# Kernel tuning notes

Measured on AMD Instinct MI355X. Metric: run time of the kernel, lower is better.

The kernel has to match this reference:

```python
import jax, jax.numpy as jnp
import numpy as np

B, W, F_IN = 128, 128, 64   # batch, window_size, num_features
N = 64                      # nodes per graph == num_features == tcn_out_channels
E = 4096                    # edges per graph
ED = 16                     # edge_feature_dim
H, C = 4, 32                # heads, gat_out_dim
FLAT = N * H * C            # 8192
HID = FLAT // 4             # 2048
LRELU_SLOPE = 0.01          # F.leaky_relu default
BN_EPS = 1e-5


def setup_inputs() -> dict:
    key = jax.random.key(0)
    ks = jax.random.split(key, 16)
    x = jax.random.normal(ks[0], (B, W, F_IN), jnp.float32)
    edge_index = jax.random.randint(ks[1], (2, E), 0, N)
    edge_attr = jax.random.normal(ks[2], (B, E, ED), jnp.float32)
    s = lambda k, shape, fan: jax.random.normal(k, shape, jnp.float32) / np.sqrt(fan)
    tcn_w = s(ks[3], (N, F_IN, 3), F_IN * 3)
    tcn_b = jnp.zeros((N,), jnp.float32)
    lin_l_w = s(ks[4], (H * C, W), W)
    lin_l_b = jnp.zeros((H * C,), jnp.float32)
    lin_e_w = s(ks[5], (H * C, ED), ED)
    lin_e_b = jnp.zeros((H * C,), jnp.float32)
    att = s(ks[6], (1, H, C), C)
    fc1_w = s(ks[7], (HID, FLAT), FLAT)
    fc1_b = jnp.zeros((HID,), jnp.float32)
    bn_g = jnp.ones((HID,), jnp.float32)
    bn_b = jnp.zeros((HID,), jnp.float32)
    fc2_w = s(ks[8], (2, HID), HID)
    fc2_b = jnp.zeros((2,), jnp.float32)
    return dict(x=x, edge_index=edge_index, edge_attr=edge_attr,
                tcn_w=tcn_w, tcn_b=tcn_b,
                lin_l_w=lin_l_w, lin_l_b=lin_l_b,
                lin_e_w=lin_e_w, lin_e_b=lin_e_b, att=att,
                fc1_w=fc1_w, fc1_b=fc1_b, bn_g=bn_g, bn_b=bn_b,
                fc2_w=fc2_w, fc2_b=fc2_b)


def reference(x, edge_index, edge_attr, tcn_w, tcn_b,
              lin_l_w, lin_l_b, lin_e_w, lin_e_b, att,
              fc1_w, fc1_b, bn_g, bn_b, fc2_w, fc2_b):
    # TCN: Conv1d(k=3, pad=1) over the window dim
    xt = jnp.transpose(x, (0, 2, 1))  # [B, F_IN, W]
    x_g = jax.lax.conv_general_dilated(
        xt, tcn_w, window_strides=(1,), padding=((1, 1),),
        dimension_numbers=('NCH', 'OIH', 'NCH')) + tcn_b[None, :, None]
    # x_g: [B, N, W] -> per-sample graph with N nodes, W-dim node features

    src, dst = edge_index[0], edge_index[1]

    def gat_one(xn, ea):
        # xn: [N, W], ea: [E, ED]
        h = (xn @ lin_l_w.T + lin_l_b).reshape(N, H, C)
        e = (ea @ lin_e_w.T + lin_e_b).reshape(E, H, C)
        xi = h[dst]               # [E, H, C] target node feats
        xj = h[src]               # [E, H, C] source node feats
        a = jax.nn.leaky_relu(xi + xj + e, LRELU_SLOPE)
        score = jnp.einsum('ehc,ohc->eh', a, att)  # [E, H]
        # segment softmax over edges grouped by destination node
        m = jax.ops.segment_max(score, dst, num_segments=N)
        m = jnp.where(jnp.isfinite(m), m, 0.0)
        ex = jnp.exp(score - m[dst])
        den = jax.ops.segment_sum(ex, dst, num_segments=N)
        alpha = ex / (den[dst] + 1e-16)            # [E, H]
        msg = xj * alpha[:, :, None]               # [E, H, C]
        out = jax.ops.segment_sum(msg, dst, num_segments=N)  # [N, H, C]
        return out.reshape(N, H * C)

    x_gat = jax.vmap(gat_one)(x_g, edge_attr)      # [B, N, H*C]
    x_gat = jax.nn.elu(x_gat)
    x_flat = x_gat.reshape(B, FLAT)

    h1 = x_flat @ fc1_w.T + fc1_b
    # BatchNorm1d in eval mode with fresh running stats (mean=0, var=1)
    h1 = h1 * (bn_g / jnp.sqrt(1.0 + BN_EPS)) + bn_b
    h1 = jax.nn.relu(h1)  # dropout is identity in eval
    logits = h1 @ fc2_w.T + fc2_b
    return logits
```

## Files before the change

### kernel.cpp

```cpp
#include <hip/hip_runtime.h>
#include <math.h>

#define BB   128
#define WW   128
#define FIN  64
#define NNODE 64
#define NE   4096
#define EDIM 16
#define NH   4
#define CDIM 32
#define HC   128
#define FLATD 8192
#define HIDD 2048

#define OFF_H    0u
#define OFF_P    1048576u
#define OFF_XGB  3211264u
#define OFF_BK   4259840u

typedef unsigned short u16;
typedef u16      u16x8 __attribute__((ext_vector_type(8)));
typedef __bf16   bf16x8 __attribute__((ext_vector_type(8)));
typedef float    f32x4  __attribute__((ext_vector_type(4)));
typedef float    f32x16 __attribute__((ext_vector_type(16)));

__device__ __forceinline__ u16 f2bf(float f) {
    unsigned u = __float_as_uint(f);
    u += 0x7fffu + ((u >> 16) & 1u);
    return (u16)(u >> 16);
}
__device__ __forceinline__ void hilo(float v, u16* h, u16* l) {
    u16 hh = f2bf(v);
    float hf = __uint_as_float(((unsigned)hh) << 16);
    *h = hh;
    *l = f2bf(v - hf);
}

__global__ __launch_bounds__(256) void k01(
        const float* __restrict__ x, const float* __restrict__ tcn_w,
        const float* __restrict__ tcn_b, const float* __restrict__ lin_l_w,
        const float* __restrict__ lin_l_b, float* __restrict__ h,
        const int* __restrict__ ei, int* __restrict__ bstart,
        int* __restrict__ blist)
{
    __shared__ float xs[130*65];
    __shared__ float xg[32*132];
    __shared__ float tw[32*192];
    __shared__ int cnt[64];
    __shared__ int cur[65];
    const int bid = blockIdx.x, t = threadIdx.x;

    if (bid == 256) {
        if (t < 64) cnt[t] = 0;
        __syncthreads();
        for (int e = t; e < NE; e += 256) atomicAdd(&cnt[ei[NE + e]], 1);
        __syncthreads();
        if (t == 0) {
            int run = 0;
            for (int n = 0; n < 64; ++n) { cur[n] = run; run += cnt[n]; }
            cur[64] = run;
        }
        __syncthreads();
        if (t < 65) bstart[t] = cur[t];
        __syncthreads();
        for (int e = t; e < NE; e += 256) {
            int d = ei[NE + e], s = ei[e];
            int p = atomicAdd(&cur[d], 1);
            blist[p] = (e << 12) | (d << 6) | s;
        }
        return;
    }

    const int b = bid >> 1, half = bid & 1;
    const int n0 = half * 32;

    for (int idx = t; idx < 8192; idx += 256) {
        int w = idx >> 6, i = idx & 63;
        xs[(w+1)*65 + i] = x[b*8192 + idx];
    }
    {
        const float4* src = (const float4*)(tcn_w + n0*192);
        for (int idx = t; idx < 1536; idx += 256)
            ((float4*)tw)[idx] = src[idx];
    }
    if (t < 65) { xs[t] = 0.f; xs[129*65 + t] = 0.f; }
    __syncthreads();

    {
        const int nl = t >> 3;
        const int n  = n0 + nl;
        const int w0 = (t & 7) * 16;
        float acc[16];
        const float tb = tcn_b[n];
#pragma unroll
        for (int j = 0; j < 16; ++j) acc[j] = tb;
        for (int i = 0; i < 64; ++i) {
            const float t0 = tw[nl*192 + 3*i + 0];
            const float t1 = tw[nl*192 + 3*i + 1];
            const float t2 = tw[nl*192 + 3*i + 2];
            float a = xs[(w0+0)*65 + i];
            float c0 = xs[(w0+1)*65 + i];
#pragma unroll
            for (int dw = 0; dw < 16; ++dw) {
                float c = xs[(w0+dw+2)*65 + i];
                acc[dw] += a*t0 + c0*t1 + c*t2;
                a = c0; c0 = c;
            }
        }
#pragma unroll
        for (int dw = 0; dw < 16; ++dw) xg[nl*132 + w0 + dw] = acc[dw];
    }
    __syncthreads();

    {
        const int o2 = t & 63, ng = t >> 6;
        const int oA = o2, oB = o2 + 64;
        float accA[8], accB[8];
        const float lbA = lin_l_b[oA], lbB = lin_l_b[oB];
#pragma unroll
        for (int j = 0; j < 8; ++j) { accA[j] = lbA; accB[j] = lbB; }
        for (int c = 0; c < 32; ++c) {
            const float4 lwA = *(const float4*)&lin_l_w[oA*128 + c*4];
            const float4 lwB = *(const float4*)&lin_l_w[oB*128 + c*4];
#pragma unroll
            for (int nn = 0; nn < 8; ++nn) {
                const float4 xv = *(const float4*)&xg[(ng*8+nn)*132 + c*4];
                accA[nn] += xv.x*lwA.x + xv.y*lwA.y + xv.z*lwA.z + xv.w*lwA.w;
                accB[nn] += xv.x*lwB.x + xv.y*lwB.y + xv.z*lwB.z + xv.w*lwB.w;
            }
        }
#pragma unroll
        for (int nn = 0; nn < 8; ++nn) {
            const int n = n0 + ng*8 + nn;
            h[(b*64 + n)*128 + oA] = accA[nn];
            h[(b*64 + n)*128 + oB] = accB[nn];
        }
    }
}

#define CAPF 2560
__global__ __launch_bounds__(512, 1) void k2_fused(
        const float* __restrict__ hbase, const float* __restrict__ ea,
        const float* __restrict__ lin_e_w, const float* __restrict__ lin_e_b,
        const float* __restrict__ att, const int* __restrict__ bstart,
        const int* __restrict__ blist, u16* __restrict__ xgb)
{
    __shared__ float hbuf[64*132];
    __shared__ float scl[CAPF*4];
    __shared__ float Pm[4][32][68];
    __shared__ int   bst[33];
    const int b = blockIdx.x, half = blockIdx.y, t = threadIdx.x;
    const int lane = t & 63, wv = t >> 6, l32 = lane & 31, h5 = lane >> 5;

    const int lo  = bstart[half*32];
    const int cnt = min(bstart[half*32 + 32] - lo, CAPF);
    const int gcnt = (cnt + 31) >> 5;

    int g = wv;
    int pkc = 0; bool validc = false;
    float4 v0c = {0.f,0.f,0.f,0.f}, v1c = {0.f,0.f,0.f,0.f};
    if (g < gcnt) {
        const int idx0 = g*32 + l32;
        validc = idx0 < cnt;
        pkc = validc ? blist[lo + idx0] : 0;
        const float* eap = ea + ((size_t)b*NE + (size_t)(pkc >> 12))*16 + h5*8;
        v0c = *(const float4*)eap;
        v1c = *(const float4*)(eap + 4);
    }

    for (int idx = t; idx < 2048; idx += 512) {
        const int row = idx >> 5, c4 = (idx & 31) * 4;
        float4 hv = *(const float4*)&hbase[(size_t)b*8192 + row*128 + c4];
        const float4 eb = *(const float4*)&lin_e_b[c4];
        hv.x += 0.5f*eb.x; hv.y += 0.5f*eb.y;
        hv.z += 0.5f*eb.z; hv.w += 0.5f*eb.w;
        *(float4*)&hbuf[row*132 + c4] = hv;
    }
    {
        const f32x4 z4 = {0.f, 0.f, 0.f, 0.f};
        for (int idx = t; idx < 4*32*68/4; idx += 512) ((f32x4*)Pm)[idx] = z4;
    }
    if (t < 33) bst[t] = bstart[half*32 + t];
    bf16x8 Ah[4], Al[4];
#pragma unroll
    for (int mt = 0; mt < 4; ++mt) {
        const float* wp = &lin_e_w[(mt*32 + l32)*16 + h5*8];
        const float4 w0 = *(const float4*)wp;
        const float4 w1 = *(const float4*)(wp + 4);
        u16 th[8], tl[8];
        hilo(w0.x,&th[0],&tl[0]); hilo(w0.y,&th[1],&tl[1]);
        hilo(w0.z,&th[2],&tl[2]); hilo(w0.w,&th[3],&tl[3]);
        hilo(w1.x,&th[4],&tl[4]); hilo(w1.y,&th[5],&tl[5]);
        hilo(w1.z,&th[6],&tl[6]); hilo(w1.w,&th[7],&tl[7]);
        u16x8 vh = { th[0],th[1],th[2],th[3],th[4],th[5],th[6],th[7] };
        u16x8 vl = { tl[0],tl[1],tl[2],tl[3],tl[4],tl[5],tl[6],tl[7] };
        Ah[mt] = *(bf16x8*)&vh;
        Al[mt] = *(bf16x8*)&vl;
    }
    float4 attv[4][4];
#pragma unroll
    for (int mt = 0; mt < 4; ++mt)
#pragma unroll
        for (int gq = 0; gq < 4; ++gq)
            attv[mt][gq] = *(const float4*)&att[mt*32 + gq*8 + h5*4];
    __syncthreads();

    while (g < gcnt) {
        const int gn = g + 8;
        const int pk = pkc; const bool valid = validc;
        const float4 v0 = v0c, v1 = v1c;
        const int idx = g*32 + l32;
        if (gn < gcnt) {
            const int idxn = gn*32 + l32;
            validc = idxn < cnt;
            pkc = validc ? blist[lo + idxn] : 0;
            const float* eap = ea + ((size_t)b*NE + (size_t)(pkc >> 12))*16 + h5*8;
            v0c = *(const float4*)eap;
            v1c = *(const float4*)(eap + 4);
        } else {
            validc = false;
        }
        const int sn = pk & 63, dd = (pk >> 6) & 63;
        u16 bh[8], bl[8];
        hilo(v0.x,&bh[0],&bl[0]); hilo(v0.y,&bh[1],&bl[1]);
        hilo(v0.z,&bh[2],&bl[2]); hilo(v0.w,&bh[3],&bl[3]);
        hilo(v1.x,&bh[4],&bl[4]); hilo(v1.y,&bh[5],&bl[5]);
        hilo(v1.z,&bh[6],&bl[6]); hilo(v1.w,&bh[7],&bl[7]);
        u16x8 vbh = { bh[0],bh[1],bh[2],bh[3],bh[4],bh[5],bh[6],bh[7] };
        u16x8 vbl = { bl[0],bl[1],bl[2],bl[3],bl[4],bl[5],bl[6],bl[7] };
        const bf16x8 Bh = *(bf16x8*)&vbh;
        const bf16x8 Bl = *(bf16x8*)&vbl;
        float hacc[4];
#pragma unroll
        for (int mt = 0; mt < 4; ++mt) {
            f32x16 D = {0.f,0.f,0.f,0.f,0.f,0.f,0.f,0.f,
                        0.f,0.f,0.f,0.f,0.f,0.f,0.f,0.f};
            D = __builtin_amdgcn_mfma_f32_32x32x16_bf16(Al[mt], Bh, D, 0, 0, 0);
            D = __builtin_amdgcn_mfma_f32_32x32x16_bf16(Ah[mt], Bl, D, 0, 0, 0);
            D = __builtin_amdgcn_mfma_f32_32x32x16_bf16(Ah[mt], Bh, D, 0, 0, 0);
            float s = 0.f;
#pragma unroll
            for (int g4 = 0; g4 < 4; ++g4) {
                const int ob = mt*32 + g4*8 + h5*4;
                const float4 hd = *(const float4*)&hbuf[dd*132 + ob];
                const float4 hs = *(const float4*)&hbuf[sn*132 + ob];
                float x0 = hd.x + hs.x + D[g4*4+0];
                float x1 = hd.y + hs.y + D[g4*4+1];
                float x2 = hd.z + hs.z + D[g4*4+2];
                float x3 = hd.w + hs.w + D[g4*4+3];
                x0 = fmaxf(x0, 0.01f*x0); x1 = fmaxf(x1, 0.01f*x1);
                x2 = fmaxf(x2, 0.01f*x2); x3 = fmaxf(x3, 0.01f*x3);
                const float4 a4 = attv[mt][g4];
                s += a4.x*x0 + a4.y*x1 + a4.z*x2 + a4.w*x3;
            }
            hacc[mt] = s;
        }
#pragma unroll
        for (int hh = 0; hh < 4; ++hh)
            hacc[hh] += __shfl_xor(hacc[hh], 32);
        if (h5 == 0 && valid)
            *(float4*)&scl[idx*4] = make_float4(hacc[0], hacc[1], hacc[2], hacc[3]);
        g = gn;
    }
    __syncthreads();

    {
        const int pair = t >> 2, sub = t & 3;
        const int nl = pair >> 2, hh = pair & 3;
        const int s0 = bst[nl] - lo, s1 = bst[nl+1] - lo;
        float mx = -3.4e38f;
        for (int i = s0 + sub; i < s1; i += 4) mx = fmaxf(mx, scl[i*4 + hh]);
        mx = fmaxf(mx, __shfl_xor(mx, 1));
        mx = fmaxf(mx, __shfl_xor(mx, 2));
        float den = 0.f;
        for (int i = s0 + sub; i < s1; i += 4) {
            const float ex = __expf(scl[i*4 + hh] - mx);
            scl[i*4 + hh] = ex;
            den += ex;
        }
        den += __shfl_xor(den, 1);
        den += __shfl_xor(den, 2);
        const float rd = 1.0f / (den + 1e-16f);
        for (int i = s0 + sub; i < s1; i += 4) {
            const int src = blist[lo + i] & 63;
            atomicAdd(&Pm[hh][nl][src], scl[i*4 + hh] * rd);
        }
    }
    __syncthreads();

    {
        const int hh = wv >> 1, ct = wv & 1;
        const int l16 = lane & 15, q = lane >> 4;
        const int cb = hh*32 + ct*16 + l16;
        const float lb2 = 0.5f * lin_e_b[cb];
        bf16x8 Hh2[2], Hl2[2];
#pragma unroll
        for (int kk = 0; kk < 2; ++kk) {
            u16 hhv[8], hlv[8];
#pragma unroll
            for (int i = 0; i < 8; ++i) {
                const float v = hbuf[(kk*32 + q*8 + i)*132 + cb];
                hilo(v, &hhv[i], &hlv[i]);
            }
            u16x8 vhh = { hhv[0],hhv[1],hhv[2],hhv[3],hhv[4],hhv[5],hhv[6],hhv[7] };
            u16x8 vhl = { hlv[0],hlv[1],hlv[2],hlv[3],hlv[4],hlv[5],hlv[6],hlv[7] };
            Hh2[kk] = *(bf16x8*)&vhh;
            Hl2[kk] = *(bf16x8*)&vhl;
        }
#pragma unroll
        for (int mrow = 0; mrow < 32; mrow += 16) {
            f32x4 D = {0.f, 0.f, 0.f, 0.f};
#pragma unroll
            for (int kk = 0; kk < 2; ++kk) {
                const float* pp = &Pm[hh][mrow + l16][kk*32 + q*8];
                const float4 a0 = *(const float4*)pp;
                const float4 a1 = *(const float4*)(pp + 4);
                u16 ph[8], pl[8];
                hilo(a0.x,&ph[0],&pl[0]); hilo(a0.y,&ph[1],&pl[1]);
                hilo(a0.z,&ph[2],&pl[2]); hilo(a0.w,&ph[3],&pl[3]);
                hilo(a1.x,&ph[4],&pl[4]); hilo(a1.y,&ph[5],&pl[5]);
                hilo(a1.z,&ph[6],&pl[6]); hilo(a1.w,&ph[7],&pl[7]);
                u16x8 vph = { ph[0],ph[1],ph[2],ph[3],ph[4],ph[5],ph[6],ph[7] };
                u16x8 vpl = { pl[0],pl[1],pl[2],pl[3],pl[4],pl[5],pl[6],pl[7] };
                const bf16x8 Ph = *(bf16x8*)&vph, Pl = *(bf16x8*)&vpl;
                D = __builtin_amdgcn_mfma_f32_16x16x32_bf16(Pl, Hh2[kk], D, 0, 0, 0);
                D = __builtin_amdgcn_mfma_f32_16x16x32_bf16(Ph, Hl2[kk], D, 0, 0, 0);
                D = __builtin_amdgcn_mfma_f32_16x16x32_bf16(Ph, Hh2[kk], D, 0, 0, 0);
            }
#pragma unroll
            for (int r = 0; r < 4; ++r) {
                const int m = mrow + q*4 + r;
                const float corr = (bst[m+1] > bst[m]) ? lb2 : 0.f;
                float v = D[r] - corr;
                v = v > 0.f ? v : expm1f(v);
                xgb[(size_t)b*8192 + (half*32 + m)*128 + cb] = f2bf(v);
            }
        }
    }
}

__global__ __launch_bounds__(256) void k3_fc1(
        const u16* __restrict__ xgb, const float* __restrict__ fc1_w,
        float* __restrict__ part)
{
    __shared__ u16 Ash[128*72];
    __shared__ u16 Bsh[32*72];
    const int jb = blockIdx.x, ks = blockIdx.y, t = threadIdx.x;
    const int j0 = jb*32, k0 = ks*1024;
    const int wave = t >> 6, lane = t & 63;
    const int quad = lane >> 4, l16 = lane & 15;
    const int wm = (wave & 1) * 64, wn = (wave >> 1) * 16;

    f32x4 acc[4];
#pragma unroll
    for (int i = 0; i < 4; ++i) acc[i] = (f32x4){0.f, 0.f, 0.f, 0.f};

    const int arow = t >> 1, acol = (t & 1) * 32;
    const int brow = t >> 3, bcol = (t & 7) * 8;

    u16x8 Ar[4]; float4 Br0, Br1;
    {
        const u16* ap = xgb + (size_t)arow*FLATD + k0 + acol;
#pragma unroll
        for (int qq = 0; qq < 4; ++qq) Ar[qq] = *(const u16x8*)(ap + qq*8);
        const float* bp = fc1_w + (size_t)(j0 + brow)*FLATD + k0 + bcol;
        Br0 = *(const float4*)bp; Br1 = *(const float4*)(bp + 4);
    }

    for (int kc = 0; kc < 1024; kc += 64) {
#pragma unroll
        for (int qq = 0; qq < 4; ++qq)
            *(u16x8*)&Ash[arow*72 + acol + qq*8] = Ar[qq];
        {
            u16x8 u = { f2bf(Br0.x), f2bf(Br0.y), f2bf(Br0.z), f2bf(Br0.w),
                        f2bf(Br1.x), f2bf(Br1.y), f2bf(Br1.z), f2bf(Br1.w) };
            *(u16x8*)&Bsh[brow*72 + bcol] = u;
        }
        __syncthreads();
        if (kc + 64 < 1024) {
            const u16* ap = xgb + (size_t)arow*FLATD + k0 + kc + 64 + acol;
#pragma unroll
            for (int qq = 0; qq < 4; ++qq) Ar[qq] = *(const u16x8*)(ap + qq*8);
            const float* bp = fc1_w + (size_t)(j0 + brow)*FLATD + k0 + kc + 64 + bcol;
            Br0 = *(const float4*)bp; Br1 = *(const float4*)(bp + 4);
        }
#pragma unroll
        for (int kk = 0; kk < 64; kk += 32) {
            bf16x8 af[4], bfr;
#pragma unroll
            for (int i = 0; i < 4; ++i)
                af[i] = *(const bf16x8*)&Ash[(wm + i*16 + l16)*72 + kk + quad*8];
            bfr = *(const bf16x8*)&Bsh[(wn + l16)*72 + kk + quad*8];
#pragma unroll
            for (int i = 0; i < 4; ++i)
                acc[i] = __builtin_amdgcn_mfma_f32_16x16x32_bf16(af[i], bfr, acc[i], 0, 0, 0);
        }
        __syncthreads();
    }
#pragma unroll
    for (int i = 0; i < 4; ++i) {
        const int n = j0 + wn + l16;
#pragma unroll
        for (int r = 0; r < 4; ++r) {
            const int m = wm + i*16 + quad*4 + r;
            part[(size_t)ks*262144 + (size_t)m*HIDD + n] = acc[i][r];
        }
    }
}

__global__ __launch_bounds__(256) void k4_fc2(
        const float* __restrict__ part, const float* __restrict__ fc1_b,
        const float* __restrict__ bn_g, const float* __restrict__ bn_b,
        const float* __restrict__ fc2_w, const float* __restrict__ fc2_b,
        float* __restrict__ out)
{
    __shared__ float r0[256], r1[256];
    const int b = blockIdx.x, t = threadIdx.x;
    const float inv = 1.0f / sqrtf(1.0f + 1e-5f);
    float p0 = 0.f, p1 = 0.f;
    for (int j = t; j < 2048; j += 256) {
        float hv = 0.f;
#pragma unroll
        for (int s = 0; s < 8; ++s) hv += part[(size_t)s*262144 + (size_t)b*2048 + j];
        float v = (hv + fc1_b[j]) * (bn_g[j] * inv) + bn_b[j];
        v = fmaxf(v, 0.f);
        p0 += v * fc2_w[j];
        p1 += v * fc2_w[2048 + j];
    }
    r0[t] = p0; r1[t] = p1;
    __syncthreads();
    for (int s = 128; s > 0; s >>= 1) {
        if (t < s) { r0[t] += r0[t+s]; r1[t] += r1[t+s]; }
        __syncthreads();
    }
    if (t == 0) {
        out[b*2 + 0] = r0[0] + fc2_b[0];
        out[b*2 + 1] = r1[0] + fc2_b[1];
    }
}

extern "C" void kernel_launch(void* const* d_in, const int* in_sizes, int n_in,
                              void* d_out, int out_size, void* d_ws, size_t ws_size,
                              hipStream_t stream)
{
    const float* x       = (const float*)d_in[0];
    const int*   ei      = (const int*)  d_in[1];
    const float* ea      = (const float*)d_in[2];
    const float* tcn_w   = (const float*)d_in[3];
    const float* tcn_b   = (const float*)d_in[4];
    const float* lin_l_w = (const float*)d_in[5];
    const float* lin_l_b = (const float*)d_in[6];
    const float* lin_e_w = (const float*)d_in[7];
    const float* lin_e_b = (const float*)d_in[8];
    const float* att     = (const float*)d_in[9];
    const float* fc1_w   = (const float*)d_in[10];
    const float* fc1_b   = (const float*)d_in[11];
    const float* bn_g    = (const float*)d_in[12];
    const float* bn_b    = (const float*)d_in[13];
    const float* fc2_w   = (const float*)d_in[14];
    const float* fc2_b   = (const float*)d_in[15];

    float* ws     = (float*)d_ws;
    float* hbuf   = ws + OFF_H;
    float* part   = ws + OFF_P;
    u16*   xgb    = (u16*)(ws + OFF_XGB);
    int*   bstart = (int*)(ws + OFF_BK);
    int*   blist  = bstart + 80;
    float* out    = (float*)d_out;

    k01    <<<257, 256, 0, stream>>>(x, tcn_w, tcn_b, lin_l_w, lin_l_b, hbuf,
                                     ei, bstart, blist);
    k2_fused<<<dim3(BB, 2), 512, 0, stream>>>(hbuf, ea, lin_e_w, lin_e_b, att,
                                              bstart, blist, xgb);
    k3_fc1 <<<dim3(64, 8), 256, 0, stream>>>(xgb, fc1_w, part);
    k4_fc2 <<<BB, 256, 0, stream>>>(part, fc1_b, bn_g, bn_b, fc2_w, fc2_b, out);
}
```

Measured before the change: 232.5 us.

## Double-buffer fc1 LDS tiles, transpose TCN weights in LDS, shuffle-reduce fc2

The fc1 GEMM now uses two LDS buffers with two register prefetch stages, so global loads and LDS writes for later tiles overlap the MFMA work on the current tile. This halves the barriers per k-step. The TCN weight tile is stored transposed in shared memory so that threads in a wave read consecutive addresses instead of strided ones. The fc2 kernel moves to 1024 threads and replaces the shared-memory tree reduction with wave shuffles followed by a small cross-wave sum. These changes cost more LDS and registers in k3, which may reduce occupancy.

```diff
diff --git a/kernel.cpp b/kernel.cpp
--- a/kernel.cpp
+++ b/kernel.cpp
@@ -45,7 +45,7 @@
 {
     __shared__ float xs[130*65];
     __shared__ float xg[32*132];
-    __shared__ float tw[32*192];
+    __shared__ float twT[192*32];
     __shared__ int cnt[64];
     __shared__ int cur[65];
     const int bid = blockIdx.x, t = threadIdx.x;
@@ -78,10 +78,9 @@
         int w = idx >> 6, i = idx & 63;
         xs[(w+1)*65 + i] = x[b*8192 + idx];
     }
-    {
-        const float4* src = (const float4*)(tcn_w + n0*192);
-        for (int idx = t; idx < 1536; idx += 256)
-            ((float4*)tw)[idx] = src[idx];
+    for (int idx = t; idx < 6144; idx += 256) {
+        const int nl = idx & 31, ik = idx >> 5;
+        twT[idx] = tcn_w[(n0 + nl)*192 + ik];
     }
     if (t < 65) { xs[t] = 0.f; xs[129*65 + t] = 0.f; }
     __syncthreads();
@@ -95,9 +94,9 @@
 #pragma unroll
         for (int j = 0; j < 16; ++j) acc[j] = tb;
         for (int i = 0; i < 64; ++i) {
-            const float t0 = tw[nl*192 + 3*i + 0];
-            const float t1 = tw[nl*192 + 3*i + 1];
-            const float t2 = tw[nl*192 + 3*i + 2];
+            const float t0 = twT[(3*i + 0)*32 + nl];
+            const float t1 = twT[(3*i + 1)*32 + nl];
+            const float t2 = twT[(3*i + 2)*32 + nl];
             float a = xs[(w0+0)*65 + i];
             float c0 = xs[(w0+1)*65 + i];
 #pragma unroll
@@ -343,8 +342,8 @@
         const u16* __restrict__ xgb, const float* __restrict__ fc1_w,
         float* __restrict__ part)
 {
-    __shared__ u16 Ash[128*72];
-    __shared__ u16 Bsh[32*72];
+    __shared__ u16 Ash[2][128*72];
+    __shared__ u16 Bsh[2][32*72];
     const int jb = blockIdx.x, ks = blockIdx.y, t = threadIdx.x;
     const int j0 = jb*32, k0 = ks*1024;
     const int wave = t >> 6, lane = t & 63;
@@ -358,45 +357,58 @@
     const int arow = t >> 1, acol = (t & 1) * 32;
     const int brow = t >> 3, bcol = (t & 7) * 8;
 
-    u16x8 Ar[4]; float4 Br0, Br1;
-    {
-        const u16* ap = xgb + (size_t)arow*FLATD + k0 + acol;
-#pragma unroll
-        for (int qq = 0; qq < 4; ++qq) Ar[qq] = *(const u16x8*)(ap + qq*8);
-        const float* bp = fc1_w + (size_t)(j0 + brow)*FLATD + k0 + bcol;
-        Br0 = *(const float4*)bp; Br1 = *(const float4*)(bp + 4);
-    }
-
-    for (int kc = 0; kc < 1024; kc += 64) {
-#pragma unroll
-        for (int qq = 0; qq < 4; ++qq)
-            *(u16x8*)&Ash[arow*72 + acol + qq*8] = Ar[qq];
-        {
-            u16x8 u = { f2bf(Br0.x), f2bf(Br0.y), f2bf(Br0.z), f2bf(Br0.w),
-                        f2bf(Br1.x), f2bf(Br1.y), f2bf(Br1.z), f2bf(Br1.w) };
-            *(u16x8*)&Bsh[brow*72 + bcol] = u;
-        }
-        __syncthreads();
-        if (kc + 64 < 1024) {
-            const u16* ap = xgb + (size_t)arow*FLATD + k0 + kc + 64 + acol;
-#pragma unroll
-            for (int qq = 0; qq < 4; ++qq) Ar[qq] = *(const u16x8*)(ap + qq*8);
-            const float* bp = fc1_w + (size_t)(j0 + brow)*FLATD + k0 + kc + 64 + bcol;
-            Br0 = *(const float4*)bp; Br1 = *(const float4*)(bp + 4);
-        }
-#pragma unroll
-        for (int kk = 0; kk < 64; kk += 32) {
-            bf16x8 af[4], bfr;
-#pragma unroll
-            for (int i = 0; i < 4; ++i)
-                af[i] = *(const bf16x8*)&Ash[(wm + i*16 + l16)*72 + kk + quad*8];
-            bfr = *(const bf16x8*)&Bsh[(wn + l16)*72 + kk + quad*8];
-#pragma unroll
-            for (int i = 0; i < 4; ++i)
-                acc[i] = __builtin_amdgcn_mfma_f32_16x16x32_bf16(af[i], bfr, acc[i], 0, 0, 0);
-        }
-        __syncthreads();
-    }
+#define K3_LOAD(KC, AR, B0, B1)                                              \
+    {   const u16* ap = xgb + (size_t)arow*FLATD + k0 + (KC) + acol;         \
+        AR[0] = *(const u16x8*)(ap);      AR[1] = *(const u16x8*)(ap + 8);   \
+        AR[2] = *(const u16x8*)(ap + 16); AR[3] = *(const u16x8*)(ap + 24);  \
+        const float* bp = fc1_w + (size_t)(j0 + brow)*FLATD + k0 + (KC) + bcol; \
+        B0 = *(const float4*)bp; B1 = *(const float4*)(bp + 4); }
+
+#define K3_WRITE(BUF, AR, B0, B1)                                            \
+    {   *(u16x8*)&Ash[BUF][arow*72 + acol]      = AR[0];                     \
+        *(u16x8*)&Ash[BUF][arow*72 + acol + 8]  = AR[1];                     \
+        *(u16x8*)&Ash[BUF][arow*72 + acol + 16] = AR[2];                     \
+        *(u16x8*)&Ash[BUF][arow*72 + acol + 24] = AR[3];                     \
+        u16x8 u = { f2bf(B0.x), f2bf(B0.y), f2bf(B0.z), f2bf(B0.w),          \
+                    f2bf(B1.x), f2bf(B1.y), f2bf(B1.z), f2bf(B1.w) };        \
+        *(u16x8*)&Bsh[BUF][brow*72 + bcol] = u; }
+
+#define K3_MFMA(BUF)                                                         \
+    {   _Pragma("unroll")                                                    \
+        for (int kk = 0; kk < 64; kk += 32) {                                \
+            bf16x8 af[4], bfr;                                               \
+            _Pragma("unroll")                                                \
+            for (int i = 0; i < 4; ++i)                                      \
+                af[i] = *(const bf16x8*)&Ash[BUF][(wm + i*16 + l16)*72 + kk + quad*8]; \
+            bfr = *(const bf16x8*)&Bsh[BUF][(wn + l16)*72 + kk + quad*8];    \
+            _Pragma("unroll")                                                \
+            for (int i = 0; i < 4; ++i)                                      \
+                acc[i] = __builtin_amdgcn_mfma_f32_16x16x32_bf16(af[i], bfr, acc[i], 0, 0, 0); \
+        } }
+
+    u16x8 Ar0[4]; float4 B00, B01;
+    u16x8 Ar1[4]; float4 B10, B11;
+
+    K3_LOAD(0, Ar0, B00, B01);
+    K3_WRITE(0, Ar0, B00, B01);
+    K3_LOAD(64, Ar0, B00, B01);
+    K3_LOAD(128, Ar1, B10, B11);
+    __syncthreads();
+
+    for (int kc = 0; kc < 1024; kc += 128) {
+        K3_MFMA(0);
+        if (kc + 64 < 1024)  K3_WRITE(1, Ar0, B00, B01);
+        if (kc + 192 < 1024) K3_LOAD(kc + 192, Ar0, B00, B01);
+        __syncthreads();
+        K3_MFMA(1);
+        if (kc + 128 < 1024) K3_WRITE(0, Ar1, B10, B11);
+        if (kc + 256 < 1024) K3_LOAD(kc + 256, Ar1, B10, B11);
+        __syncthreads();
+    }
+#undef K3_LOAD
+#undef K3_WRITE
+#undef K3_MFMA
+
 #pragma unroll
     for (int i = 0; i < 4; ++i) {
         const int n = j0 + wn + l16;
@@ -408,17 +420,20 @@
     }
 }
 
-__global__ __launch_bounds__(256) void k4_fc2(
+__global__ __launch_bounds__(1024) void k4_fc2(
         const float* __restrict__ part, const float* __restrict__ fc1_b,
         const float* __restrict__ bn_g, const float* __restrict__ bn_b,
         const float* __restrict__ fc2_w, const float* __restrict__ fc2_b,
         float* __restrict__ out)
 {
-    __shared__ float r0[256], r1[256];
+    __shared__ float w0s[16], w1s[16];
     const int b = blockIdx.x, t = threadIdx.x;
+    const int lane = t & 63, wv = t >> 6;
     const float inv = 1.0f / sqrtf(1.0f + 1e-5f);
     float p0 = 0.f, p1 = 0.f;
-    for (int j = t; j < 2048; j += 256) {
+#pragma unroll
+    for (int jj = 0; jj < 2; ++jj) {
+        const int j = t + jj*1024;
         float hv = 0.f;
 #pragma unroll
         for (int s = 0; s < 8; ++s) hv += part[(size_t)s*262144 + (size_t)b*2048 + j];
@@ -427,15 +442,19 @@
         p0 += v * fc2_w[j];
         p1 += v * fc2_w[2048 + j];
     }
-    r0[t] = p0; r1[t] = p1;
-    __syncthreads();
-    for (int s = 128; s > 0; s >>= 1) {
-        if (t < s) { r0[t] += r0[t+s]; r1[t] += r1[t+s]; }
-        __syncthreads();
-    }
+#pragma unroll
+    for (int d = 1; d < 64; d <<= 1) {
+        p0 += __shfl_xor(p0, d);
+        p1 += __shfl_xor(p1, d);
+    }
+    if (lane == 0) { w0s[wv] = p0; w1s[wv] = p1; }
+    __syncthreads();
     if (t == 0) {
-        out[b*2 + 0] = r0[0] + fc2_b[0];
-        out[b*2 + 1] = r1[0] + fc2_b[1];
+        float s0 = 0.f, s1 = 0.f;
+#pragma unroll
+        for (int i = 0; i < 16; ++i) { s0 += w0s[i]; s1 += w1s[i]; }
+        out[b*2 + 0] = s0 + fc2_b[0];
+        out[b*2 + 1] = s1 + fc2_b[1];
     }
 }
 
@@ -473,5 +492,5 @@
     k2_fused<<<dim3(BB, 2), 512, 0, stream>>>(hbuf, ea, lin_e_w, lin_e_b, att,
                                               bstart, blist, xgb);
     k3_fc1 <<<dim3(64, 8), 256, 0, stream>>>(xgb, fc1_w, part);
-    k4_fc2 <<<BB, 256, 0, stream>>>(part, fc1_b, bn_g, bn_b, fc2_w, fc2_b, out);
-}
+    k4_fc2 <<<BB, 1024, 0, stream>>>(part, fc1_b, bn_g, bn_b, fc2_w, fc2_b, out);
+}
```

Measured after the change: 232.3 us. About the same (-0.1%).
